# Kernel optimization log

Measured on AMD Instinct MI355X. Metric: run time of the kernel, lower is better.

The kernel has to match this reference:

```python
import math
import jax, jax.numpy as jnp
import numpy as np

B, N, D = 2, 768, 512
H = 8
DK = D // H
BETA_NOT = 0.5
EPS = 1e-6


def setup_inputs() -> dict:
    key = jax.random.key(0)
    ks = jax.random.split(key, 8)
    s = 0.02
    return {
        "x": jax.random.normal(ks[0], (B, N, D), dtype=jnp.float32),
        "qkv1_w": jax.random.normal(ks[1], (D, 3 * D), dtype=jnp.float32) * s,
        "qkv2_w": jax.random.normal(ks[2], (D, 3 * D), dtype=jnp.float32) * s,
        "proj_w": jax.random.normal(ks[3], (D, D), dtype=jnp.float32) * s,
        "conv1_w": jax.random.normal(ks[4], (16, 6), dtype=jnp.float32) * 0.3,
        "conv1_b": jax.random.normal(ks[5], (16,), dtype=jnp.float32) * 0.1,
        "conv2_w": jax.random.normal(ks[6], (4, 16), dtype=jnp.float32) * 0.3,
        "conv2_b": jnp.full((4,), -5.0, dtype=jnp.float32),
        "chain_logit": jnp.asarray(-2.0, dtype=jnp.float32),
    }


def _qkv(x, w):
    b, n, d = x.shape
    qkv = (x @ w).reshape(b, n, 3, H, DK).transpose(2, 0, 3, 1, 4)  # [3,B,h,N,dk]
    return qkv[0], qkv[1], qkv[2]


def reference(x, qkv1_w, qkv2_w, proj_w, conv1_w, conv1_b, conv2_w, conv2_b, chain_logit):
    scale = 1.0 / math.sqrt(DK)
    q1, k1, v1 = _qkv(x, qkv1_w)
    q2, k2, v2 = _qkv(x, qkv2_w)

    S1 = jnp.einsum("bhnd,bhmd->bhnm", q1, k1) * scale  # [B,h,N,N]
    S2 = jnp.einsum("bhnd,bhmd->bhnm", q2, k2) * scale
    A1 = jax.nn.softmax(S1, axis=-1)
    A2 = jax.nn.softmax(S2, axis=-1)

    C_right = jnp.einsum("bhnk,bhkm->bhnm", A1, A2)
    C_left = jnp.einsum("bhnk,bhkm->bhnm", A2, A1)
    Cr = jnp.log(C_right + EPS)
    Cl = jnp.log(C_left + EPS)

    # 6-channel edge feature map [B,h,6,N,N]
    feat = jnp.stack(
        [S1, S2, jnp.swapaxes(S1, -1, -2), jnp.swapaxes(S2, -1, -2), Cr, Cl], axis=2
    )
    # 1x1 convs == per-pixel channel mixing
    hid = jnp.einsum("bhcnm,oc->bhonm", feat, conv1_w) + conv1_b[None, None, :, None, None]
    hid = jax.nn.gelu(hid, approximate=True)  # tanh-approx GELU
    gates = jax.nn.sigmoid(
        jnp.einsum("bhcnm,oc->bhonm", hid, conv2_w) + conv2_b[None, None, :, None, None]
    )
    g_and, g_or, g_not, g_chain = gates[:, :, 0], gates[:, :, 1], gates[:, :, 2], gates[:, :, 3]

    Smix = (
        S1
        + g_and * S2  # g_and * (S1 + S2 - S1)
        + g_or * (jnp.logaddexp(S1, S2) - S1)
        - g_not * (BETA_NOT * S2)
        + g_chain * Cr
    )
    A = jax.nn.softmax(Smix, axis=-1)

    y_base = jnp.einsum("bhnm,bhmd->bhnd", A, v1)
    transport = jnp.einsum("bhnm,bhmd->bhnd", A2, v2)
    y_chain = jnp.einsum("bhnm,bhmd->bhnd", A1, transport)
    w = jax.nn.sigmoid(chain_logit)
    y = y_base + w * y_chain

    y = jnp.swapaxes(y, 1, 2).reshape(x.shape[0], x.shape[1], D)  # [B,N,D]
    return y @ proj_w
```

## Files before the change

kernel.cpp:

```cpp
#include <hip/hip_runtime.h>
#include <hip/hip_bf16.h>
#include <math.h>

typedef __hip_bfloat16 bf16;
typedef __attribute__((ext_vector_type(8))) short short8;
typedef __attribute__((ext_vector_type(4))) float f32x4;
typedef __attribute__((ext_vector_type(2))) float f32x2;
#define DEVINL __device__ __forceinline__

constexpr int Bc  = 2;
constexpr int Nc  = 768;
constexpr int Dc  = 512;
constexpr int Hc  = 8;
constexpr int DKc = 64;
constexpr int BHc = Bc * Hc;
constexpr float SCALE    = 0.125f;
constexpr float EPSF     = 1e-6f;
constexpr float BETA_NOT = 0.5f;

DEVINL float ldf(const float* p, long i) { return p[i]; }
DEVINL float ldf(const bf16* p, long i) { return __bfloat162float(p[i]); }
DEVINL void stf(float* p, long i, float v) { p[i] = v; }
DEVINL void stf(bf16* p, long i, float v) { p[i] = __float2bfloat16(v); }

DEVINL float sigf(float x) { return __fdividef(1.f, 1.f + __expf(-x)); }

DEVINL f32x2 fma2(f32x2 a, f32x2 b, f32x2 c) { return __builtin_elementwise_fma(a, b, c); }
DEVINL f32x2 splat2(float x) { return (f32x2){x, x}; }
DEVINL float vexp2(float x) { float r; asm("v_exp_f32 %0, %1" : "=v"(r) : "v"(x)); return r; }
DEVINL float vrcp(float x)  { float r; asm("v_rcp_f32 %0, %1" : "=v"(r) : "v"(x)); return r; }
DEVINL float vlog2(float x) { float r; asm("v_log_f32 %0, %1" : "=v"(r) : "v"(x)); return r; }

DEVINL void gl_lds16(const void* g, void* l) {
    __builtin_amdgcn_global_load_lds(
        (const __attribute__((address_space(1))) void*)g,
        (__attribute__((address_space(3))) void*)l, 16, 0, 0);
}

DEVINL int sniff_is_fp32(const void* xraw) {
    const uint4* p4 = (const uint4*)xraw;
    float mx = 0.f;
#pragma unroll
    for (int j = 0; j < 16; ++j) {
        const uint4 u = p4[j];
        const unsigned w[4] = {u.x, u.y, u.z, u.w};
#pragma unroll
        for (int t = 0; t < 4; ++t) {
            mx = fmaxf(mx, fabsf(__uint_as_float((w[t] & 0xffffu) << 16)));
            mx = fmaxf(mx, fabsf(__uint_as_float(w[t] & 0xffff0000u)));
        }
    }
    return mx > 1000.f ? 1 : 0;
}

DEVINL float cvt_elem(const void* s, long j, int is32) {
    return is32 ? ((const float*)s)[j]
                : __bfloat162float(((const bf16*)s)[j]);
}

__global__ __launch_bounds__(256) void convert_all(
    const void* x, const void* w1, const void* w2, const void* pw,
    const void* c1w, const void* c1b, const void* c2w, const void* c2b,
    const void* ch,
    bf16* xb, bf16* w1b, bf16* w2b, bf16* pwb, float* smallf)
{
    __shared__ int is32s;
    if (threadIdx.x == 0) is32s = sniff_is_fp32(x);
    __syncthreads();
    const int is32 = is32s;
    const long i = (long)blockIdx.x * 256 + threadIdx.x;
    if (i < (long)Bc * Nc * Dc) {
        xb[i]  = __float2bfloat16(cvt_elem(x,  i, is32));
        w1b[i] = __float2bfloat16(cvt_elem(w1, i, is32));
        w2b[i] = __float2bfloat16(cvt_elem(w2, i, is32));
    }
    if (i < (long)Dc * Dc) pwb[i] = __float2bfloat16(cvt_elem(pw, i, is32));
    if (i < 384) {
        const int u = (int)i / 24, k = (int)i % 24;
        float v = 0.f;
        if (k < 12)      v = cvt_elem(c1w, u * 6 + (k >> 1), is32);
        else if (k < 14) v = cvt_elem(c1b, u, is32);
        else if (k >= 16) { const int o = (k - 16) >> 1; v = cvt_elem(c2w, o * 16 + u, is32); }
        smallf[i] = v;
    } else if (i < 392) smallf[i] = cvt_elem(c2b, ((int)i - 384) >> 1, is32);
    else if (i < 394) smallf[i] = cvt_elem(ch, 0, is32);
    else if (i < 512) smallf[i] = 0.f;
}

__global__ __launch_bounds__(256) void fill_sentinel(unsigned short* o) {
    const long i = (long)blockIdx.x * 256 + threadIdx.x;
    if (i < (long)Bc * Nc * Dc) o[i] = 0x40E0;
}

__global__ __launch_bounds__(256) void transpose_bf16(
    const unsigned short* __restrict__ src, unsigned short* __restrict__ dst,
    int R, int C, long sS, long sD)
{
    __shared__ unsigned short tile[64][68];
    const unsigned short* s = src + (long)blockIdx.z * sS;
    unsigned short* d = dst + (long)blockIdx.z * sD;
    const int r0 = blockIdx.y * 64, c0 = blockIdx.x * 64;
    const int t = threadIdx.x;
    const int lr = t >> 4, lc4 = (t & 15) * 4;
#pragma unroll
    for (int i = 0; i < 4; ++i) {
        int r = lr + i * 16;
        *(uint2*)&tile[r][lc4] = *(const uint2*)&s[(long)(r0 + r) * C + c0 + lc4];
    }
    __syncthreads();
#pragma unroll
    for (int i = 0; i < 4; ++i) {
        int r = lr + i * 16;
        unsigned short v[4];
#pragma unroll
        for (int j = 0; j < 4; ++j) v[j] = tile[lc4 + j][r];
        *(uint2*)&d[(long)(c0 + r) * R + r0 + lc4] = *(uint2*)v;
    }
}

template <int EPI, typename TC, int XORB = 0, int XCDSWZ = 0, int RAW = 0>
__global__ __launch_bounds__(256) void gemm_nt_mfma(
    const bf16* __restrict__ Ag, const bf16* __restrict__ Btg,
    TC* __restrict__ Cg, bf16* __restrict__ Craw, int M, int N, int K,
    long sA, long sB, long sC, float alpha)
{
    __shared__ unsigned short Asm[2 * 128 * 32];
    __shared__ unsigned short Bsm[2 * 128 * 32];
    constexpr int BUF = 128 * 32;

    int bx, by, bz;
    if (XCDSWZ) {
        const int wg = blockIdx.x;
        const int xcd = wg & 7, t = wg >> 3;
        bz = xcd + 8 * (t / 36);
        const int tile = t % 36;
        bx = tile % 6; by = tile / 6;
    } else { bx = blockIdx.x; by = blockIdx.y; bz = blockIdx.z; }

    const int tid  = threadIdx.x;
    const int wv   = tid >> 6;
    const int lane = tid & 63;
    const int q    = lane >> 4;
    const int ln   = lane & 15;
    const int wm   = wv & 1;
    const int wn   = wv >> 1;

    const int zb = XORB ? (bz ^ 16) : bz;
    const bf16* A  = Ag  + (long)bz * sA + (long)(by * 128) * K;
    const bf16* Bt = Btg + (long)zb * sB + (long)(bx * 128) * K;
    TC*         C  = Cg  + (long)bz * sC;

    const int sr = lane >> 2, sc = lane & 3;
    const int scs = sc ^ (sr & 3);
    const bf16* gA0 = A  + (long)(wv * 32 + sr)      * K + scs * 8;
    const bf16* gA1 = A  + (long)(wv * 32 + 16 + sr) * K + scs * 8;
    const bf16* gB0 = Bt + (long)(wv * 32 + sr)      * K + scs * 8;
    const bf16* gB1 = Bt + (long)(wv * 32 + 16 + sr) * K + scs * 8;
    unsigned short* lA0 = &Asm[(wv * 32)      * 32];
    unsigned short* lA1 = &Asm[(wv * 32 + 16) * 32];
    unsigned short* lB0 = &Bsm[(wv * 32)      * 32];
    unsigned short* lB1 = &Bsm[(wv * 32 + 16) * 32];

    f32x4 acc[4][4];
#pragma unroll
    for (int i = 0; i < 4; ++i)
#pragma unroll
        for (int j = 0; j < 4; ++j)
            acc[i][j] = (f32x4){0.f, 0.f, 0.f, 0.f};

    const int qs = (q ^ (ln & 3)) * 8;

    gl_lds16(gA0, lA0);
    gl_lds16(gA1, lA1);
    gl_lds16(gB0, lB0);
    gl_lds16(gB1, lB1);
    __syncthreads();

    int cur = 0;
    for (int k0 = 0; k0 < K; k0 += 32) {
        const int nxt = cur ^ 1;
        if (k0 + 32 < K) {
            const int no = nxt * BUF;
            gl_lds16(gA0 + k0 + 32, lA0 + no);
            gl_lds16(gA1 + k0 + 32, lA1 + no);
            gl_lds16(gB0 + k0 + 32, lB0 + no);
            gl_lds16(gB1 + k0 + 32, lB1 + no);
        }

        const unsigned short* Ac = &Asm[cur * BUF];
        const unsigned short* Bc = &Bsm[cur * BUF];
        short8 af[4], bfr[4];
#pragma unroll
        for (int mt = 0; mt < 4; ++mt) {
            int m = wm * 64 + mt * 16 + ln;
            af[mt] = *(const short8*)&Ac[m * 32 + qs];
        }
#pragma unroll
        for (int nt = 0; nt < 4; ++nt) {
            int n = wn * 64 + nt * 16 + ln;
            bfr[nt] = *(const short8*)&Bc[n * 32 + qs];
        }
#pragma unroll
        for (int mt = 0; mt < 4; ++mt)
#pragma unroll
            for (int nt = 0; nt < 4; ++nt)
                acc[mt][nt] = __builtin_amdgcn_mfma_f32_16x16x32_bf16(
                    af[mt], bfr[nt], acc[mt][nt], 0, 0, 0);

        __syncthreads();
        cur = nxt;
    }

#pragma unroll
    for (int mt = 0; mt < 4; ++mt) {
#pragma unroll
        for (int nt = 0; nt < 4; ++nt) {
            const int col = bx * 128 + wn * 64 + nt * 16 + ln;
            const int rowb = by * 128 + wm * 64 + mt * 16 + q * 4;
#pragma unroll
            for (int r = 0; r < 4; ++r) {
                float vraw = acc[mt][nt][r] * alpha;
                if (RAW) {
                    if (bz < 16)
                        Craw[(long)bz * M * N + (long)(rowb + r) * N + col] =
                            __float2bfloat16(vraw);
                }
                float v = vraw;
                if (EPI == 1) v = __logf(fmaxf(v, 0.f) + EPSF);
                stf(C, (long)(rowb + r) * N + col, v);
            }
        }
    }
}

__global__ __launch_bounds__(256) void qkv_mfma(
    const bf16* __restrict__ X,
    const bf16* __restrict__ w1t, const bf16* __restrict__ w2t,
    bf16* __restrict__ q1, bf16* __restrict__ k1, bf16* __restrict__ v1,
    bf16* __restrict__ q2, bf16* __restrict__ k2, bf16* __restrict__ v2)
{
    constexpr int K = Dc;
    __shared__ unsigned short Asm[2 * 128 * 32];
    __shared__ unsigned short Bsm[2 * 128 * 32];
    constexpr int BUF = 128 * 32;

    const int tid  = threadIdx.x;
    const int wv   = tid >> 6;
    const int lane = tid & 63;
    const int q    = lane >> 4;
    const int ln   = lane & 15;
    const int wm   = wv & 1;
    const int wn   = wv >> 1;
    const int set  = blockIdx.z;

    const bf16* Wt = set ? w2t : w1t;
    bf16* Q  = set ? q2 : q1;
    bf16* Ko = set ? k2 : k1;
    bf16* V  = set ? v2 : v1;

    const bf16* A  = X  + (long)(blockIdx.y * 128) * K;
    const bf16* Bt = Wt + (long)(blockIdx.x * 128) * K;

    const int sr = lane >> 2, sc = lane & 3;
    const int scs = sc ^ (sr & 3);
    const bf16* gA0 = A  + (long)(wv * 32 + sr)      * K + scs * 8;
    const bf16* gA1 = A  + (long)(wv * 32 + 16 + sr) * K + scs * 8;
    const bf16* gB0 = Bt + (long)(wv * 32 + sr)      * K + scs * 8;
    const bf16* gB1 = Bt + (long)(wv * 32 + 16 + sr) * K + scs * 8;
    unsigned short* lA0 = &Asm[(wv * 32)      * 32];
    unsigned short* lA1 = &Asm[(wv * 32 + 16) * 32];
    unsigned short* lB0 = &Bsm[(wv * 32)      * 32];
    unsigned short* lB1 = &Bsm[(wv * 32 + 16) * 32];

    f32x4 acc[4][4];
#pragma unroll
    for (int i = 0; i < 4; ++i)
#pragma unroll
        for (int j = 0; j < 4; ++j)
            acc[i][j] = (f32x4){0.f, 0.f, 0.f, 0.f};

    const int qs = (q ^ (ln & 3)) * 8;

    gl_lds16(gA0, lA0);
    gl_lds16(gA1, lA1);
    gl_lds16(gB0, lB0);
    gl_lds16(gB1, lB1);
    __syncthreads();

    int cur = 0;
    for (int k0 = 0; k0 < K; k0 += 32) {
        const int nxt = cur ^ 1;
        if (k0 + 32 < K) {
            const int no = nxt * BUF;
            gl_lds16(gA0 + k0 + 32, lA0 + no);
            gl_lds16(gA1 + k0 + 32, lA1 + no);
            gl_lds16(gB0 + k0 + 32, lB0 + no);
            gl_lds16(gB1 + k0 + 32, lB1 + no);
        }

        const unsigned short* Ac = &Asm[cur * BUF];
        const unsigned short* Bc = &Bsm[cur * BUF];
        short8 af[4], bfr[4];
#pragma unroll
        for (int mt = 0; mt < 4; ++mt) {
            int m = wm * 64 + mt * 16 + ln;
            af[mt] = *(const short8*)&Ac[m * 32 + qs];
        }
#pragma unroll
        for (int nt = 0; nt < 4; ++nt) {
            int n = wn * 64 + nt * 16 + ln;
            bfr[nt] = *(const short8*)&Bc[n * 32 + qs];
        }
#pragma unroll
        for (int mt = 0; mt < 4; ++mt)
#pragma unroll
            for (int nt = 0; nt < 4; ++nt)
                acc[mt][nt] = __builtin_amdgcn_mfma_f32_16x16x32_bf16(
                    af[mt], bfr[nt], acc[mt][nt], 0, 0, 0);

        __syncthreads();
        cur = nxt;
    }

#pragma unroll
    for (int mt = 0; mt < 4; ++mt) {
#pragma unroll
        for (int nt = 0; nt < 4; ++nt) {
            const int col  = blockIdx.x * 128 + wn * 64 + nt * 16 + ln;
            const int rowb = blockIdx.y * 128 + wm * 64 + mt * 16 + q * 4;
            const int t = col >> 9;
            const int h = (col >> 6) & 7;
            const int dk = col & 63;
            bf16* dst = (t == 0) ? Q : (t == 1) ? Ko : V;
#pragma unroll
            for (int r = 0; r < 4; ++r) {
                const int row = rowb + r;
                const int b = row >= Nc ? 1 : 0;
                const int n = row - b * Nc;
                dst[(((long)b * Hc + h) * Nc + n) * DKc + dk] =
                    __float2bfloat16(acc[mt][nt][r]);
            }
        }
    }
}

struct N64Acc { f32x4 acc[2][4]; };

template <typename DUMMY = void>
DEVINL void n64_core(const bf16* A, const bf16* Bt, int K,
                     unsigned short* Asm, unsigned short* Bsm, N64Acc& R)
{
    const int tid  = threadIdx.x;
    const int wave = tid >> 6;
    const int lane = tid & 63;
    const int q    = lane >> 4;
    const int ln   = lane & 15;

    const int sr = tid >> 3, k8 = tid & 7;
    const bf16* pa[4];
    const bf16* pb[2];
    int wa[4], wb[2];
#pragma unroll
    for (int i = 0; i < 4; ++i) {
        pa[i] = A + (long)(sr + i * 32) * K + k8 * 8;
        wa[i] = (sr + i * 32) * 72 + k8 * 8;
    }
#pragma unroll
    for (int i = 0; i < 2; ++i) {
        pb[i] = Bt + (long)(sr + i * 32) * K + k8 * 8;
        wb[i] = (sr + i * 32) * 72 + k8 * 8;
    }

#pragma unroll
    for (int i = 0; i < 2; ++i)
#pragma unroll
        for (int j = 0; j < 4; ++j)
            R.acc[i][j] = (f32x4){0.f, 0.f, 0.f, 0.f};

    for (int k0 = 0; k0 < K; k0 += 64) {
        uint4 va[4], vb[2];
#pragma unroll
        for (int i = 0; i < 4; ++i) va[i] = *(const uint4*)(pa[i] + k0);
#pragma unroll
        for (int i = 0; i < 2; ++i) vb[i] = *(const uint4*)(pb[i] + k0);
        __syncthreads();
#pragma unroll
        for (int i = 0; i < 4; ++i) *(uint4*)&Asm[wa[i]] = va[i];
#pragma unroll
        for (int i = 0; i < 2; ++i) *(uint4*)&Bsm[wb[i]] = vb[i];
        __syncthreads();

#pragma unroll
        for (int kc = 0; kc < 2; ++kc) {
            short8 af[2], bfr[4];
#pragma unroll
            for (int mt = 0; mt < 2; ++mt) {
                int m = wave * 32 + mt * 16 + ln;
                af[mt] = *(const short8*)&Asm[m * 72 + kc * 32 + q * 8];
            }
#pragma unroll
            for (int nt = 0; nt < 4; ++nt) {
                int n = nt * 16 + ln;
                bfr[nt] = *(const short8*)&Bsm[n * 72 + kc * 32 + q * 8];
            }
#pragma unroll
            for (int mt = 0; mt < 2; ++mt)
#pragma unroll
                for (int nt = 0; nt < 4; ++nt)
                    R.acc[mt][nt] = __builtin_amdgcn_mfma_f32_16x16x32_bf16(
                        af[mt], bfr[nt], R.acc[mt][nt], 0, 0, 0);
        }
    }
}

__global__ __launch_bounds__(256) void gemm_n64_pair(
    const bf16* __restrict__ A0g, const bf16* __restrict__ B0g, bf16* __restrict__ C0tg,
    const bf16* __restrict__ A1g, const bf16* __restrict__ B1g, bf16* __restrict__ C1g,
    int M, int K, long sA, long sB, long sC)
{
    __shared__ unsigned short Asm[128 * 72];
    __shared__ unsigned short Bsm[64 * 72];

    const int zz = blockIdx.z & 15;
    const int second = blockIdx.z >> 4;
    const bf16* A  = (second ? A1g : A0g) + (long)zz * sA + (long)(blockIdx.y * 128) * K;
    const bf16* Bt = (second ? B1g : B0g) + (long)zz * sB;

    N64Acc R;
    n64_core(A, Bt, K, Asm, Bsm, R);

    const int tid = threadIdx.x;
    const int wave = tid >> 6, lane = tid & 63, q = lane >> 4, ln = lane & 15;

    if (second) {
        bf16* C = C1g + (long)zz * sC;
#pragma unroll
        for (int mt = 0; mt < 2; ++mt) {
#pragma unroll
            for (int nt = 0; nt < 4; ++nt) {
                const int col  = nt * 16 + ln;
                const int rowb = blockIdx.y * 128 + wave * 32 + mt * 16 + q * 4;
#pragma unroll
                for (int r = 0; r < 4; ++r)
                    C[(long)(rowb + r) * 64 + col] = __float2bfloat16(R.acc[mt][nt][r]);
            }
        }
    } else {
        __syncthreads();
#pragma unroll
        for (int mt = 0; mt < 2; ++mt) {
#pragma unroll
            for (int nt = 0; nt < 4; ++nt) {
                const int col = nt * 16 + ln;
                const int rwb = wave * 32 + mt * 16 + q * 4;
#pragma unroll
                for (int r = 0; r < 4; ++r)
                    *(bf16*)&Asm[col * 136 + rwb + r] = __float2bfloat16(R.acc[mt][nt][r]);
            }
        }
        __syncthreads();
        bf16* Ct = C0tg + (long)zz * sC;
        const int dk  = tid >> 2;
        const int nc0 = (tid & 3) * 32;
        const int gn0 = blockIdx.y * 128;
#pragma unroll
        for (int c8 = 0; c8 < 4; ++c8) {
            uint4 v = *(const uint4*)&Asm[dk * 136 + nc0 + c8 * 8];
            *(uint4*)&Ct[(long)dk * Nc + gn0 + nc0 + c8 * 8] = v;
        }
    }
}

__global__ __launch_bounds__(256) void gemm_n64_yb(
    const bf16* __restrict__ Ag, const bf16* __restrict__ Btg,
    bf16* __restrict__ Cg, int M, int K, long sA, long sB, long sC)
{
    __shared__ unsigned short Asm[128 * 72];
    __shared__ unsigned short Bsm[64 * 72];

    const int zz = blockIdx.z;
    const bf16* A  = Ag + (long)zz * sA + (long)(blockIdx.y * 128) * K;
    const bf16* Bt = Btg + (long)zz * sB;

    N64Acc R;
    n64_core(A, Bt, K, Asm, Bsm, R);

    bf16* C = Cg + (long)zz * sC;
    const int tid = threadIdx.x;
    const int wave = tid >> 6, lane = tid & 63, q = lane >> 4, ln = lane & 15;
#pragma unroll
    for (int mt = 0; mt < 2; ++mt) {
#pragma unroll
        for (int nt = 0; nt < 4; ++nt) {
            const int col  = nt * 16 + ln;
            const int rowb = blockIdx.y * 128 + wave * 32 + mt * 16 + q * 4;
#pragma unroll
            for (int r = 0; r < 4; ++r)
                C[(long)(rowb + r) * 64 + col] = __float2bfloat16(R.acc[mt][nt][r]);
        }
    }
}

__global__ __launch_bounds__(256) void gemm_n64_combine(
    const bf16* __restrict__ A1b, const bf16* __restrict__ trt,
    const bf16* __restrict__ yb1, const float* __restrict__ smallf,
    bf16* __restrict__ yc, int M, int K, long sA, long sB)
{
    __shared__ unsigned short Asm[128 * 72];
    __shared__ unsigned short Bsm[64 * 72];

    const int bh = blockIdx.z;
    const bf16* A  = A1b + (long)bh * sA + (long)(blockIdx.y * 128) * K;
    const bf16* Bt = trt + (long)bh * sB;

    N64Acc R;
    n64_core(A, Bt, K, Asm, Bsm, R);

    const float w = sigf(smallf[392]);
    const int b = bh >> 3, h = bh & 7;
    const long yb1base = (long)bh * Nc * DKc;

    const int tid = threadIdx.x;
    const int wave = tid >> 6, lane = tid & 63, q = lane >> 4, ln = lane & 15;
#pragma unroll
    for (int mt = 0; mt < 2; ++mt) {
#pragma unroll
        for (int nt = 0; nt < 4; ++nt) {
            const int col  = nt * 16 + ln;
            const int rowb = blockIdx.y * 128 + wave * 32 + mt * 16 + q * 4;
#pragma unroll
            for (int r = 0; r < 4; ++r) {
                const int n = rowb + r;
                const float base = __bfloat162float(yb1[yb1base + (long)n * 64 + col]);
                yc[((long)(b * Nc + n)) * Dc + h * DKc + col] =
                    __float2bfloat16(base + w * R.acc[mt][nt][r]);
            }
        }
    }
}

__global__ __launch_bounds__(256) void softmax_rows_w(
    const float* __restrict__ src, bf16* __restrict__ dst)
{
    const int wid  = threadIdx.x >> 6;
    const int lane = threadIdx.x & 63;
    const long row = (long)blockIdx.x * 4 + wid;
    const float* s = src + row * Nc;

    float4 v[3];
#pragma unroll
    for (int i = 0; i < 3; ++i)
        v[i] = *(const float4*)&s[i * 256 + lane * 4];

    float m = -1e30f;
#pragma unroll
    for (int i = 0; i < 3; ++i)
        m = fmaxf(m, fmaxf(fmaxf(v[i].x, v[i].y), fmaxf(v[i].z, v[i].w)));
#pragma unroll
    for (int off = 32; off > 0; off >>= 1)
        m = fmaxf(m, __shfl_xor(m, off, 64));

    float e[12];
    float sum = 0.f;
#pragma unroll
    for (int i = 0; i < 3; ++i) {
        e[i * 4 + 0] = __expf(v[i].x - m);
        e[i * 4 + 1] = __expf(v[i].y - m);
        e[i * 4 + 2] = __expf(v[i].z - m);
        e[i * 4 + 3] = __expf(v[i].w - m);
        sum += e[i * 4 + 0] + e[i * 4 + 1] + e[i * 4 + 2] + e[i * 4 + 3];
    }
#pragma unroll
    for (int off = 32; off > 0; off >>= 1)
        sum += __shfl_xor(sum, off, 64);

    const float inv = 1.f / fmaxf(sum, 1e-30f);
    unsigned short* d = (unsigned short*)dst + row * Nc;
#pragma unroll
    for (int i = 0; i < 3; ++i) {
        unsigned short o[4];
#pragma unroll
        for (int j = 0; j < 4; ++j) {
            const bf16 b = __float2bfloat16(e[i * 4 + j] * inv);
            o[j] = *(const unsigned short*)&b;
        }
        *(uint2*)&d[i * 256 + lane * 4] = *(const uint2*)o;
    }
}

__global__ __launch_bounds__(256) void gates_smix(
    const float* __restrict__ S1g, const float* __restrict__ S2g,
    const bf16* __restrict__ Crg, const bf16* __restrict__ Clg,
    float* __restrict__ Smixg, const float* __restrict__ smallf)
{
    __shared__ float t1t[32][17], t2t[32][17];

    const long mat = (long)blockIdx.z * Nc * Nc;
    const float* S1 = S1g + mat;
    const float* S2 = S2g + mat;
    const unsigned short* Cr = (const unsigned short*)Crg + mat;
    const unsigned short* Cl = (const unsigned short*)Clg + mat;
    float* Smix = Smixg + mat;

    const int tid = threadIdx.x;

    const int n0 = blockIdx.y * 16, m0 = blockIdx.x * 32;
    {
        const int r = tid >> 3, c2 = (tid & 7) * 2;
        const float2 a = *(const float2*)&S1[(long)(m0 + r) * Nc + n0 + c2];
        const float2 b = *(const float2*)&S2[(long)(m0 + r) * Nc + n0 + c2];
        t1t[r][c2] = a.x; t1t[r][c2 + 1] = a.y;
        t2t[r][c2] = b.x; t2t[r][c2 + 1] = b.y;
    }
    __syncthreads();

    const int tx = tid & 15, ty = tid >> 4;
    const int n = n0 + ty;
    const long idx = (long)n * Nc + m0 + tx * 2;

    const float2 s1v = *(const float2*)&S1[idx];
    const float2 s2v = *(const float2*)&S2[idx];
    const unsigned cru = *(const unsigned*)&Cr[idx];
    const unsigned clu = *(const unsigned*)&Cl[idx];

    const f32x2 s1a = {s1v.x, s1v.y};
    const f32x2 s2a = {s2v.x, s2v.y};
    const f32x2 cra = {__uint_as_float((cru & 0xffffu) << 16),
                       __uint_as_float(cru & 0xffff0000u)};
    const f32x2 cla = {__uint_as_float((clu & 0xffffu) << 16),
                       __uint_as_float(clu & 0xffff0000u)};
    const f32x2 s1t = {t1t[tx * 2][ty], t1t[tx * 2 + 1][ty]};
    const f32x2 s2t = {t2t[tx * 2][ty], t2t[tx * 2 + 1][ty]};

    f32x2 g0 = *(const f32x2*)&smallf[384];
    f32x2 g1 = *(const f32x2*)&smallf[386];
    f32x2 g2 = *(const f32x2*)&smallf[388];
    f32x2 g3 = *(const f32x2*)&smallf[390];

    const f32x2 gc1  = splat2(-2.30220902f);
    const f32x2 gc3  = splat2(-0.10294357f);
    const f32x2 one2 = splat2(1.f);

#pragma unroll
    for (int u = 0; u < 16; ++u) {
        const f32x2* cw = (const f32x2*)&smallf[u * 24];
        f32x2 h = cw[6];
        h = fma2(s1a, cw[0], h);
        h = fma2(s2a, cw[1], h);
        h = fma2(s1t, cw[2], h);
        h = fma2(s2t, cw[3], h);
        h = fma2(cra, cw[4], h);
        h = fma2(cla, cw[5], h);
        const f32x2 hh = h * h;
        const f32x2 z2 = h * fma2(hh, gc3, gc1);
        f32x2 e;  e[0]  = vexp2(z2[0]); e[1]  = vexp2(z2[1]);
        const f32x2 d = one2 + e;
        f32x2 rc; rc[0] = vrcp(d[0]);   rc[1] = vrcp(d[1]);
        const f32x2 hid = h * rc;
        g0 = fma2(hid, cw[8],  g0);
        g1 = fma2(hid, cw[9],  g1);
        g2 = fma2(hid, cw[10], g2);
        g3 = fma2(hid, cw[11], g3);
    }

    const f32x2 nl2e = splat2(-1.44269504f);
    const f32x2 ln2v = splat2(0.69314718f);
    auto sig2 = [&](f32x2 x) -> f32x2 {
        const f32x2 t = x * nl2e;
        f32x2 e;  e[0] = vexp2(t[0]); e[1] = vexp2(t[1]);
        const f32x2 d = one2 + e;
        f32x2 r;  r[0] = vrcp(d[0]);  r[1] = vrcp(d[1]);
        return r;
    };
    const f32x2 ga2 = sig2(g0);
    const f32x2 go2 = sig2(g1);
    const f32x2 gn2 = sig2(g2);
    const f32x2 gc2 = sig2(g3);

    const f32x2 dd = s1a - s2a;
    f32x2 ad; ad[0] = fabsf(dd[0]); ad[1] = fabsf(dd[1]);
    const f32x2 t2 = ad * nl2e;
    f32x2 ee; ee[0] = vexp2(t2[0]); ee[1] = vexp2(t2[1]);
    const f32x2 lp = one2 + ee;
    f32x2 lg; lg[0] = vlog2(lp[0]); lg[1] = vlog2(lp[1]);
    const f32x2 mx2 = __builtin_elementwise_max(s1a, s2a);
    const f32x2 lae = fma2(lg, ln2v, mx2);

    f32x2 o2 = s1a;
    o2 = fma2(ga2, s2a, o2);
    o2 = fma2(go2, lae - s1a, o2);
    o2 = fma2(gn2, s2a * splat2(-BETA_NOT), o2);
    o2 = fma2(gc2, cra, o2);
    *(float2*)&Smix[idx] = (float2){o2[0], o2[1]};
}

__global__ __launch_bounds__(256) void proj_n64(
    const bf16* __restrict__ yc, const bf16* __restrict__ pwt,
    const void* __restrict__ xraw, void* __restrict__ out)
{
    constexpr int K = Dc;
    constexpr int N = Dc;
    __shared__ unsigned short Asm[128 * 72];
    __shared__ unsigned short Bsm[64 * 72];
    __shared__ int is32s;
    if (threadIdx.x == 0) is32s = sniff_is_fp32(xraw);

    const bf16* A  = yc  + (long)(blockIdx.y * 128) * K;
    const bf16* Bt = pwt + (long)(blockIdx.x * 64) * K;

    N64Acc R;
    n64_core(A, Bt, K, Asm, Bsm, R);

    const int is32 = is32s;
    const int tid = threadIdx.x;
    const int wave = tid >> 6, lane = tid & 63, q = lane >> 4, ln = lane & 15;
#pragma unroll
    for (int mt = 0; mt < 2; ++mt) {
#pragma unroll
        for (int nt = 0; nt < 4; ++nt) {
            const int col  = blockIdx.x * 64 + nt * 16 + ln;
            const int rowb = blockIdx.y * 128 + wave * 32 + mt * 16 + q * 4;
#pragma unroll
            for (int r = 0; r < 4; ++r) {
                const long o = (long)(rowb + r) * N + col;
                if (is32) ((float*)out)[o] = R.acc[mt][nt][r];
                else      ((bf16*)out)[o] = __float2bfloat16(R.acc[mt][nt][r]);
            }
        }
    }
}

extern "C" void kernel_launch(void* const* d_in, const int* in_sizes, int n_in,
                              void* d_out, int out_size, void* d_ws, size_t ws_size,
                              hipStream_t stream)
{
    const size_t HD   = (size_t)BHc * Nc * DKc;
    const size_t HDh  = HD / 2;
    const size_t MAT  = (size_t)Nc * Nc;
    const size_t MATS = (size_t)BHc * MAT;
    const long   HSTR = (long)Nc * DKc;

    float* ws = (float*)d_ws;
    size_t off = 0;
    auto alloc = [&](size_t n) { float* p = ws + off; off += n; return p; };

    bf16* xb  = (bf16*)alloc(HDh);
    bf16* w1b = (bf16*)alloc(HDh);
    bf16* w2b = (bf16*)alloc(HDh);
    bf16* w1t = (bf16*)alloc(HDh);
    bf16* w2t = (bf16*)alloc(HDh);
    bf16* pwb = (bf16*)alloc((size_t)Dc * Dc / 2);
    bf16* pwt = (bf16*)alloc((size_t)Dc * Dc / 2);
    float* smallf = alloc(512);
    bf16* q1b = (bf16*)alloc(HDh); bf16* q2b = (bf16*)alloc(HDh);
    bf16* k1b = (bf16*)alloc(HDh); bf16* k2b = (bf16*)alloc(HDh);
    bf16* v1b = (bf16*)alloc(HDh); bf16* v2b = (bf16*)alloc(HDh);
    bf16* v1t = (bf16*)alloc(HDh); bf16* v2t = (bf16*)alloc(HDh);
    bf16* trt = (bf16*)alloc(HDh);
    float* S1   = alloc(MATS);
    float* S2   = alloc(MATS);
    float* Smix = alloc(MATS);
    bf16* A1b = (bf16*)alloc(MATS / 2);
    bf16* A2b = (bf16*)alloc(MATS / 2);
    bf16* Crb = (bf16*)alloc(MATS / 2);
    bf16* Clb = (bf16*)alloc(MATS / 2);
    bf16* yb1 = (bf16*)alloc(HDh);
    bf16* yc  = (bf16*)alloc(HDh);

    const size_t NEED_BASE = off * sizeof(float);
    bf16* Crawb = (bf16*)alloc(MATS / 2);
    const size_t NEED_A = off * sizeof(float);
    const int pathA = ws_size >= NEED_A;

    bf16* A1tb = (bf16*)Smix;
    bf16* A2tb = ((bf16*)Smix) + MATS;
    bf16* Ab   = (bf16*)S1;

    if (ws_size < NEED_BASE) {
        fill_sentinel<<<dim3(3072), 256, 0, stream>>>((unsigned short*)d_out);
        return;
    }

    convert_all<<<dim3(3072), 256, 0, stream>>>(
        d_in[0], d_in[1], d_in[2], d_in[3], d_in[4], d_in[5], d_in[6], d_in[7],
        d_in[8], xb, w1b, w2b, pwb, smallf);

    transpose_bf16<<<dim3(24, 8, 2), 256, 0, stream>>>(
        (const unsigned short*)w1b, (unsigned short*)w1t, Dc, 3 * Dc, (long)HD, (long)HD);
    transpose_bf16<<<dim3(8, 8, 1), 256, 0, stream>>>(
        (const unsigned short*)pwb, (unsigned short*)pwt, Dc, Dc, 0, 0);
    qkv_mfma<<<dim3(12, 12, 2), 256, 0, stream>>>(
        xb, w1t, w2t, q1b, k1b, v1b, q2b, k2b, v2b);
    transpose_bf16<<<dim3(1, 12, 2 * BHc), 256, 0, stream>>>(
        (const unsigned short*)v1b, (unsigned short*)v1t, Nc, DKc, HSTR, HSTR);

    gemm_nt_mfma<0, float><<<dim3(6, 6, 2 * BHc), 256, 0, stream>>>(
        q1b, k1b, S1, nullptr, Nc, Nc, DKc, HSTR, HSTR, (long)MAT, SCALE);

    softmax_rows_w<<<(2 * BHc * Nc) / 4, 256, 0, stream>>>(S1, A1b);
    transpose_bf16<<<dim3(12, 12, 2 * BHc), 256, 0, stream>>>(
        (const unsigned short*)A1b, (unsigned short*)A1tb, Nc, Nc, (long)MAT, (long)MAT);

    if (pathA)
        gemm_nt_mfma<1, bf16, 1, 1, 1><<<dim3(1152), 256, 0, stream>>>(
            A1b, A1tb, Crb, Crawb, Nc, Nc, Nc, (long)MAT, (long)MAT, (long)MAT, 1.f);
    else
        gemm_nt_mfma<1, bf16, 1, 1, 0><<<dim3(1152), 256, 0, stream>>>(
            A1b, A1tb, Crb, nullptr, Nc, Nc, Nc, (long)MAT, (long)MAT, (long)MAT, 1.f);

    gates_smix<<<dim3(24, 48, BHc), 256, 0, stream>>>(S1, S2, Crb, Clb, Smix, smallf);

    softmax_rows_w<<<(BHc * Nc) / 4, 256, 0, stream>>>(Smix, Ab);

    if (pathA) {
        gemm_n64_yb<<<dim3(1, 6, BHc), 256, 0, stream>>>(
            Ab, v1t, yb1, Nc, Nc, (long)MAT, HSTR, HSTR);
        gemm_n64_combine<<<dim3(1, 6, BHc), 256, 0, stream>>>(
            Crawb, v2t, yb1, smallf, yc, Nc, Nc, (long)MAT, HSTR);
    } else {
        gemm_n64_pair<<<dim3(1, 6, 2 * BHc), 256, 0, stream>>>(
            A2b, v2t, trt, Ab, v1t, yb1, Nc, Nc, (long)MAT, HSTR, HSTR);
        gemm_n64_combine<<<dim3(1, 6, BHc), 256, 0, stream>>>(
            A1b, trt, yb1, smallf, yc, Nc, Nc, (long)MAT, HSTR);
    }

    proj_n64<<<dim3(8, 12, 1), 256, 0, stream>>>(yc, pwt, d_in[0], d_out);
}
```

Measured before the change: 383.4 us.

## Fuse yb and combine GEMMs into one kernel; widen gates_smix per-thread work

On pathA, the two separate kernels that compute A·v1 into a scratch buffer and then add w times Craw·v2 are merged into one kernel. It runs both GEMMs back to back in the same block and writes the combined result straight to yc. This drops a launch and the round trip through the yb1 buffer, but the grid stays small (96 blocks) and each block now does twice the serial work. Separately, gates_smix now handles four columns per thread instead of two, with float4 loads and stores and half the grid, which gives more ILP per thread at the cost of more registers.

```diff
diff --git a/kernel.cpp b/kernel.cpp
--- a/kernel.cpp
+++ b/kernel.cpp
@@ -471,21 +471,26 @@
     }
 }
 
-__global__ __launch_bounds__(256) void gemm_n64_yb(
-    const bf16* __restrict__ Ag, const bf16* __restrict__ Btg,
-    bf16* __restrict__ Cg, int M, int K, long sA, long sB, long sC)
+__global__ __launch_bounds__(256) void gemm_n64_both(
+    const bf16* __restrict__ Ab, const bf16* __restrict__ v1t,
+    const bf16* __restrict__ Craw, const bf16* __restrict__ v2t,
+    const float* __restrict__ smallf, bf16* __restrict__ yc,
+    int K, long sA, long sB)
 {
     __shared__ unsigned short Asm[128 * 72];
     __shared__ unsigned short Bsm[64 * 72];
 
-    const int zz = blockIdx.z;
-    const bf16* A  = Ag + (long)zz * sA + (long)(blockIdx.y * 128) * K;
-    const bf16* Bt = Btg + (long)zz * sB;
-
-    N64Acc R;
-    n64_core(A, Bt, K, Asm, Bsm, R);
-
-    bf16* C = Cg + (long)zz * sC;
+    const int bh = blockIdx.z;
+    const long arow = (long)(blockIdx.y * 128) * K;
+
+    N64Acc R1;
+    n64_core(Ab + (long)bh * sA + arow, v1t + (long)bh * sB, K, Asm, Bsm, R1);
+    N64Acc R2;
+    n64_core(Craw + (long)bh * sA + arow, v2t + (long)bh * sB, K, Asm, Bsm, R2);
+
+    const float w = sigf(smallf[392]);
+    const int b = bh >> 3, h = bh & 7;
+
     const int tid = threadIdx.x;
     const int wave = tid >> 6, lane = tid & 63, q = lane >> 4, ln = lane & 15;
 #pragma unroll
@@ -495,8 +500,11 @@
             const int col  = nt * 16 + ln;
             const int rowb = blockIdx.y * 128 + wave * 32 + mt * 16 + q * 4;
 #pragma unroll
-            for (int r = 0; r < 4; ++r)
-                C[(long)(rowb + r) * 64 + col] = __float2bfloat16(R.acc[mt][nt][r]);
+            for (int r = 0; r < 4; ++r) {
+                const int n = rowb + r;
+                yc[((long)(b * Nc + n)) * Dc + h * DKc + col] =
+                    __float2bfloat16(R1.acc[mt][nt][r] + w * R2.acc[mt][nt][r]);
+            }
         }
     }
 }
@@ -539,6 +547,36 @@
     }
 }
 
+__global__ __launch_bounds__(256) void gemm_n64_yb(
+    const bf16* __restrict__ Ag, const bf16* __restrict__ Btg,
+    bf16* __restrict__ Cg, int M, int K, long sA, long sB, long sC)
+{
+    __shared__ unsigned short Asm[128 * 72];
+    __shared__ unsigned short Bsm[64 * 72];
+
+    const int zz = blockIdx.z;
+    const bf16* A  = Ag + (long)zz * sA + (long)(blockIdx.y * 128) * K;
+    const bf16* Bt = Btg + (long)zz * sB;
+
+    N64Acc R;
+    n64_core(A, Bt, K, Asm, Bsm, R);
+
+    bf16* C = Cg + (long)zz * sC;
+    const int tid = threadIdx.x;
+    const int wave = tid >> 6, lane = tid & 63, q = lane >> 4, ln = lane & 15;
+#pragma unroll
+    for (int mt = 0; mt < 2; ++mt) {
+#pragma unroll
+        for (int nt = 0; nt < 4; ++nt) {
+            const int col  = nt * 16 + ln;
+            const int rowb = blockIdx.y * 128 + wave * 32 + mt * 16 + q * 4;
+#pragma unroll
+            for (int r = 0; r < 4; ++r)
+                C[(long)(rowb + r) * 64 + col] = __float2bfloat16(R.acc[mt][nt][r]);
+        }
+    }
+}
+
 __global__ __launch_bounds__(256) void softmax_rows_w(
     const float* __restrict__ src, bf16* __restrict__ dst)
 {
@@ -593,7 +631,7 @@
     const bf16* __restrict__ Crg, const bf16* __restrict__ Clg,
     float* __restrict__ Smixg, const float* __restrict__ smallf)
 {
-    __shared__ float t1t[32][17], t2t[32][17];
+    __shared__ float t1t[64][17], t2t[64][17];
 
     const long mat = (long)blockIdx.z * Nc * Nc;
     const float* S1 = S1g + mat;
@@ -604,38 +642,50 @@
 
     const int tid = threadIdx.x;
 
-    const int n0 = blockIdx.y * 16, m0 = blockIdx.x * 32;
+    const int n0 = blockIdx.y * 16, m0 = blockIdx.x * 64;
     {
-        const int r = tid >> 3, c2 = (tid & 7) * 2;
-        const float2 a = *(const float2*)&S1[(long)(m0 + r) * Nc + n0 + c2];
-        const float2 b = *(const float2*)&S2[(long)(m0 + r) * Nc + n0 + c2];
-        t1t[r][c2] = a.x; t1t[r][c2 + 1] = a.y;
-        t2t[r][c2] = b.x; t2t[r][c2 + 1] = b.y;
+        const int r = tid >> 2, c4 = (tid & 3) * 4;
+        const float4 a = *(const float4*)&S1[(long)(m0 + r) * Nc + n0 + c4];
+        const float4 b = *(const float4*)&S2[(long)(m0 + r) * Nc + n0 + c4];
+        t1t[r][c4] = a.x; t1t[r][c4 + 1] = a.y; t1t[r][c4 + 2] = a.z; t1t[r][c4 + 3] = a.w;
+        t2t[r][c4] = b.x; t2t[r][c4 + 1] = b.y; t2t[r][c4 + 2] = b.z; t2t[r][c4 + 3] = b.w;
     }
     __syncthreads();
 
     const int tx = tid & 15, ty = tid >> 4;
     const int n = n0 + ty;
-    const long idx = (long)n * Nc + m0 + tx * 2;
-
-    const float2 s1v = *(const float2*)&S1[idx];
-    const float2 s2v = *(const float2*)&S2[idx];
-    const unsigned cru = *(const unsigned*)&Cr[idx];
-    const unsigned clu = *(const unsigned*)&Cl[idx];
-
-    const f32x2 s1a = {s1v.x, s1v.y};
-    const f32x2 s2a = {s2v.x, s2v.y};
-    const f32x2 cra = {__uint_as_float((cru & 0xffffu) << 16),
-                       __uint_as_float(cru & 0xffff0000u)};
-    const f32x2 cla = {__uint_as_float((clu & 0xffffu) << 16),
-                       __uint_as_float(clu & 0xffff0000u)};
-    const f32x2 s1t = {t1t[tx * 2][ty], t1t[tx * 2 + 1][ty]};
-    const f32x2 s2t = {t2t[tx * 2][ty], t2t[tx * 2 + 1][ty]};
-
-    f32x2 g0 = *(const f32x2*)&smallf[384];
-    f32x2 g1 = *(const f32x2*)&smallf[386];
-    f32x2 g2 = *(const f32x2*)&smallf[388];
-    f32x2 g3 = *(const f32x2*)&smallf[390];
+    const long idx = (long)n * Nc + m0 + tx * 4;
+
+    const float4 s1v = *(const float4*)&S1[idx];
+    const float4 s2v = *(const float4*)&S2[idx];
+    const uint2 cru = *(const uint2*)&Cr[idx];
+    const uint2 clu = *(const uint2*)&Cl[idx];
+
+    f32x2 s1a[2] = {{s1v.x, s1v.y}, {s1v.z, s1v.w}};
+    f32x2 s2a[2] = {{s2v.x, s2v.y}, {s2v.z, s2v.w}};
+    f32x2 cra[2] = {{__uint_as_float((cru.x & 0xffffu) << 16),
+                     __uint_as_float(cru.x & 0xffff0000u)},
+                    {__uint_as_float((cru.y & 0xffffu) << 16),
+                     __uint_as_float(cru.y & 0xffff0000u)}};
+    f32x2 cla[2] = {{__uint_as_float((clu.x & 0xffffu) << 16),
+                     __uint_as_float(clu.x & 0xffff0000u)},
+                    {__uint_as_float((clu.y & 0xffffu) << 16),
+                     __uint_as_float(clu.y & 0xffff0000u)}};
+    f32x2 s1t[2], s2t[2];
+#pragma unroll
+    for (int p = 0; p < 2; ++p) {
+        s1t[p] = (f32x2){t1t[tx * 4 + 2 * p][ty], t1t[tx * 4 + 2 * p + 1][ty]};
+        s2t[p] = (f32x2){t2t[tx * 4 + 2 * p][ty], t2t[tx * 4 + 2 * p + 1][ty]};
+    }
+
+    f32x2 g0[2], g1[2], g2[2], g3[2];
+#pragma unroll
+    for (int p = 0; p < 2; ++p) {
+        g0[p] = *(const f32x2*)&smallf[384];
+        g1[p] = *(const f32x2*)&smallf[386];
+        g2[p] = *(const f32x2*)&smallf[388];
+        g3[p] = *(const f32x2*)&smallf[390];
+    }
 
     const f32x2 gc1  = splat2(-2.30220902f);
     const f32x2 gc3  = splat2(-0.10294357f);
@@ -644,23 +694,26 @@
 #pragma unroll
     for (int u = 0; u < 16; ++u) {
         const f32x2* cw = (const f32x2*)&smallf[u * 24];
-        f32x2 h = cw[6];
-        h = fma2(s1a, cw[0], h);
-        h = fma2(s2a, cw[1], h);
-        h = fma2(s1t, cw[2], h);
-        h = fma2(s2t, cw[3], h);
-        h = fma2(cra, cw[4], h);
-        h = fma2(cla, cw[5], h);
-        const f32x2 hh = h * h;
-        const f32x2 z2 = h * fma2(hh, gc3, gc1);
-        f32x2 e;  e[0]  = vexp2(z2[0]); e[1]  = vexp2(z2[1]);
-        const f32x2 d = one2 + e;
-        f32x2 rc; rc[0] = vrcp(d[0]);   rc[1] = vrcp(d[1]);
-        const f32x2 hid = h * rc;
-        g0 = fma2(hid, cw[8],  g0);
-        g1 = fma2(hid, cw[9],  g1);
-        g2 = fma2(hid, cw[10], g2);
-        g3 = fma2(hid, cw[11], g3);
+#pragma unroll
+        for (int p = 0; p < 2; ++p) {
+            f32x2 h = cw[6];
+            h = fma2(s1a[p], cw[0], h);
+            h = fma2(s2a[p], cw[1], h);
+            h = fma2(s1t[p], cw[2], h);
+            h = fma2(s2t[p], cw[3], h);
+            h = fma2(cra[p], cw[4], h);
+            h = fma2(cla[p], cw[5], h);
+            const f32x2 hh = h * h;
+            const f32x2 z2 = h * fma2(hh, gc3, gc1);
+            f32x2 e;  e[0]  = vexp2(z2[0]); e[1]  = vexp2(z2[1]);
+            const f32x2 d = one2 + e;
+            f32x2 rc; rc[0] = vrcp(d[0]);   rc[1] = vrcp(d[1]);
+            const f32x2 hid = h * rc;
+            g0[p] = fma2(hid, cw[8],  g0[p]);
+            g1[p] = fma2(hid, cw[9],  g1[p]);
+            g2[p] = fma2(hid, cw[10], g2[p]);
+            g3[p] = fma2(hid, cw[11], g3[p]);
+        }
     }
 
     const f32x2 nl2e = splat2(-1.44269504f);
@@ -672,26 +725,34 @@
         f32x2 r;  r[0] = vrcp(d[0]);  r[1] = vrcp(d[1]);
         return r;
     };
-    const f32x2 ga2 = sig2(g0);
-    const f32x2 go2 = sig2(g1);
-    const f32x2 gn2 = sig2(g2);
-    const f32x2 gc2 = sig2(g3);
-
-    const f32x2 dd = s1a - s2a;
-    f32x2 ad; ad[0] = fabsf(dd[0]); ad[1] = fabsf(dd[1]);
-    const f32x2 t2 = ad * nl2e;
-    f32x2 ee; ee[0] = vexp2(t2[0]); ee[1] = vexp2(t2[1]);
-    const f32x2 lp = one2 + ee;
-    f32x2 lg; lg[0] = vlog2(lp[0]); lg[1] = vlog2(lp[1]);
-    const f32x2 mx2 = __builtin_elementwise_max(s1a, s2a);
-    const f32x2 lae = fma2(lg, ln2v, mx2);
-
-    f32x2 o2 = s1a;
-    o2 = fma2(ga2, s2a, o2);
-    o2 = fma2(go2, lae - s1a, o2);
-    o2 = fma2(gn2, s2a * splat2(-BETA_NOT), o2);
-    o2 = fma2(gc2, cra, o2);
-    *(float2*)&Smix[idx] = (float2){o2[0], o2[1]};
+
+    float4 outv;
+    float* outp = &outv.x;
+#pragma unroll
+    for (int p = 0; p < 2; ++p) {
+        const f32x2 ga2 = sig2(g0[p]);
+        const f32x2 go2 = sig2(g1[p]);
+        const f32x2 gn2 = sig2(g2[p]);
+        const f32x2 gc2 = sig2(g3[p]);
+
+        const f32x2 dd = s1a[p] - s2a[p];
+        f32x2 ad; ad[0] = fabsf(dd[0]); ad[1] = fabsf(dd[1]);
+        const f32x2 t2 = ad * nl2e;
+        f32x2 ee; ee[0] = vexp2(t2[0]); ee[1] = vexp2(t2[1]);
+        const f32x2 lp = one2 + ee;
+        f32x2 lg; lg[0] = vlog2(lp[0]); lg[1] = vlog2(lp[1]);
+        const f32x2 mx2 = __builtin_elementwise_max(s1a[p], s2a[p]);
+        const f32x2 lae = fma2(lg, ln2v, mx2);
+
+        f32x2 o2 = s1a[p];
+        o2 = fma2(ga2, s2a[p], o2);
+        o2 = fma2(go2, lae - s1a[p], o2);
+        o2 = fma2(gn2, s2a[p] * splat2(-BETA_NOT), o2);
+        o2 = fma2(gc2, cra[p], o2);
+        outp[2 * p]     = o2[0];
+        outp[2 * p + 1] = o2[1];
+    }
+    *(float4*)&Smix[idx] = outv;
 }
 
 __global__ __launch_bounds__(256) void proj_n64(
@@ -808,15 +869,13 @@
         gemm_nt_mfma<1, bf16, 1, 1, 0><<<dim3(1152), 256, 0, stream>>>(
             A1b, A1tb, Crb, nullptr, Nc, Nc, Nc, (long)MAT, (long)MAT, (long)MAT, 1.f);
 
-    gates_smix<<<dim3(24, 48, BHc), 256, 0, stream>>>(S1, S2, Crb, Clb, Smix, smallf);
+    gates_smix<<<dim3(12, 48, BHc), 256, 0, stream>>>(S1, S2, Crb, Clb, Smix, smallf);
 
     softmax_rows_w<<<(BHc * Nc) / 4, 256, 0, stream>>>(Smix, Ab);
 
     if (pathA) {
-        gemm_n64_yb<<<dim3(1, 6, BHc), 256, 0, stream>>>(
-            Ab, v1t, yb1, Nc, Nc, (long)MAT, HSTR, HSTR);
-        gemm_n64_combine<<<dim3(1, 6, BHc), 256, 0, stream>>>(
-            Crawb, v2t, yb1, smallf, yc, Nc, Nc, (long)MAT, HSTR);
+        gemm_n64_both<<<dim3(1, 6, BHc), 256, 0, stream>>>(
+            Ab, v1t, Crawb, v2t, smallf, yc, Nc, (long)MAT, HSTR);
     } else {
         gemm_n64_pair<<<dim3(1, 6, 2 * BHc), 256, 0, stream>>>(
             A2b, v2t, trt, Ab, v1t, yb1, Nc, Nc, (long)MAT, HSTR, HSTR);
```

After: 369.0 us. 1.04x faster.
